# Optimization experiments

Hardware: AMD Instinct MI355X
Metric: run time of the kernel (lower is better)

Reference implementation:

```python
import jax, jax.numpy as jnp
import numpy as np

N_NODES = 50000
N_EDGES = 800000
LATDIM = 128
HEAD = 4


def setup_inputs() -> dict:
    key = jax.random.key(0)
    k1, k2, k3, k4, k5, k6 = jax.random.split(key, 6)
    scale = 1.0 / np.sqrt(LATDIM)  # xavier-ish scale for the square projections
    return {
        "embeds": jax.random.normal(k1, (N_NODES, LATDIM), dtype=jnp.float32),
        "qW": jax.random.normal(k2, (LATDIM, LATDIM), dtype=jnp.float32) * scale,
        "kW": jax.random.normal(k3, (LATDIM, LATDIM), dtype=jnp.float32) * scale,
        "vW": jax.random.normal(k4, (LATDIM, LATDIM), dtype=jnp.float32) * scale,
        "rows": jax.random.randint(k5, (N_EDGES,), 0, N_NODES, dtype=jnp.int32),
        "cols": jax.random.randint(k6, (N_EDGES,), 0, N_NODES, dtype=jnp.int32),
    }


def reference(embeds, qW, kW, vW, rows, cols):
    n_nodes, latdim = embeds.shape
    head_dim = latdim // HEAD
    rowEmb = embeds[rows]                         # [E, D] gather by dst
    colEmb = embeds[cols]                         # [E, D] gather by src
    q = (rowEmb @ qW).reshape(-1, HEAD, head_dim)  # [E, H, Dh]
    k = (colEmb @ kW).reshape(-1, HEAD, head_dim)
    v = (colEmb @ vW).reshape(-1, HEAD, head_dim)
    att = jnp.einsum('ehd,ehd->eh', q, k)
    att = jnp.clip(att, -10.0, 10.0)
    expAtt = jnp.exp(att)                          # [E, H]
    # segment softmax denominator via scatter-add over destination nodes
    attNorm = jax.ops.segment_sum(expAtt, rows, num_segments=n_nodes)[rows]
    att = expAtt / (attNorm + 1e-8)
    res = (att[:, :, None] * v).reshape(-1, latdim)  # [E, D]
    out = jax.ops.segment_sum(res, rows, num_segments=n_nodes)  # [N, D]
    return out
```

## Files before the change

### kernel.cpp

```cpp
#include <hip/hip_runtime.h>
#include <hip/hip_bf16.h>

#define N_NODES 50000
#define N_EDGES 800000
#define LATDIM 128
#define HEAD 4
#define SLOT_CAP 96

typedef __attribute__((ext_vector_type(8))) short short8;
typedef __attribute__((ext_vector_type(4))) float floatx4;

__device__ __forceinline__ unsigned bf16_rne_bits(float x) {
    unsigned u = __builtin_bit_cast(unsigned, x);
    return (u + 0x7fffu + ((u >> 16) & 1u)) & 0xffff0000u;
}
__device__ __forceinline__ void split_bf16(float x, short& hi, short& lo) {
    unsigned hb = bf16_rne_bits(x);
    hi = (short)(hb >> 16);
    float hf = __builtin_bit_cast(float, hb);
    unsigned lb = bf16_rne_bits(x - hf);
    lo = (short)(lb >> 16);
}

#define SCAT_BLOCKS ((N_EDGES / 4 + 255) / 256)

__global__ __launch_bounds__(256) void prep_kernel(
    const float* __restrict__ qW, const float* __restrict__ kW,
    const float* __restrict__ vW,
    short* __restrict__ Whi, short* __restrict__ Wlo,
    const int* __restrict__ rows, const int* __restrict__ cols,
    int* __restrict__ cnt, int* __restrict__ slots)
{
    const int b = blockIdx.x;
    if (b < 192) {
        const int which = b >> 6;
        const float* W = (which == 0) ? qW : (which == 1) ? kW : vW;
        const int t = (b & 63) * 256 + threadIdx.x;
        const int k = t >> 7, n = t & 127;
        const int c = k >> 5, q = (k >> 3) & 3, j = k & 7;
        short hi, lo;
        split_bf16(W[k * 128 + n], hi, lo);
        const int dst = which * 16384 + ((c * 128 + n) * 4 + q) * 8 + j;
        Whi[dst] = hi;
        Wlo[dst] = lo;
    } else {
        const int t = (b - 192) * 256 + threadIdx.x;
        if (t < N_EDGES / 4) {
            int4 r = ((const int4*)rows)[t];
            int4 c = ((const int4*)cols)[t];
            int p;
            p = atomicAdd(&cnt[r.x], 1);
            if (p < SLOT_CAP) slots[(size_t)r.x * SLOT_CAP + p] = c.x;
            p = atomicAdd(&cnt[r.y], 1);
            if (p < SLOT_CAP) slots[(size_t)r.y * SLOT_CAP + p] = c.y;
            p = atomicAdd(&cnt[r.z], 1);
            if (p < SLOT_CAP) slots[(size_t)r.z * SLOT_CAP + p] = c.z;
            p = atomicAdd(&cnt[r.w], 1);
            if (p < SLOT_CAP) slots[(size_t)r.w * SLOT_CAP + p] = c.w;
        }
    }
}

#define GEMM_BLOCKS ((N_NODES + 63) / 64)
#define LDSP 136

__global__ __launch_bounds__(768) void gemm_kernel(
    const float* __restrict__ E,
    const short* __restrict__ Whi, const short* __restrict__ Wlo,
    float* __restrict__ Q, unsigned short* __restrict__ KV2)
{
    __shared__ short AhL[64 * LDSP];
    __shared__ short AlL[64 * LDSP];

    const int r_base = blockIdx.x * 64;

    for (int chnk = threadIdx.x; chnk < 2048; chnk += 768) {
        const int row = chnk >> 5, c4 = chnk & 31;
        int grow = r_base + row;
        if (grow > N_NODES - 1) grow = N_NODES - 1;
        float4 x = ((const float4*)E)[(size_t)grow * 32 + c4];
        short h0, l0, h1, l1, h2, l2, h3, l3;
        split_bf16(x.x, h0, l0);
        split_bf16(x.y, h1, l1);
        split_bf16(x.z, h2, l2);
        split_bf16(x.w, h3, l3);
        *(short4*)(AhL + row * LDSP + c4 * 4) = make_short4(h0, h1, h2, h3);
        *(short4*)(AlL + row * LDSP + c4 * 4) = make_short4(l0, l1, l2, l3);
    }
    __syncthreads();

    const int wave = threadIdx.x >> 6;
    const int lane = threadIdx.x & 63;
    const int which = wave >> 2;
    const int n_base = (wave & 3) * 32;
    const int ln = lane & 15;
    const int q  = lane >> 4;

    short8 Bh[2][4], Bl[2][4];
#pragma unroll
    for (int tIdx = 0; tIdx < 2; ++tIdx)
#pragma unroll
        for (int c = 0; c < 4; ++c) {
            const int off = which * 16384 +
                            ((c * 128 + n_base + tIdx * 16 + ln) * 4 + q) * 8;
            Bh[tIdx][c] = *(const short8*)(Whi + off);
            Bl[tIdx][c] = *(const short8*)(Wlo + off);
        }

    const int vs = (which == 2) ? 32 : 0;
    const int c0 = n_base + ln;
    const int c1 = n_base + 16 + ln;

    for (int rt = 0; rt < 4; ++rt) {
        const short* ah = AhL + (rt * 16 + ln) * LDSP + q * 8;
        const short* al = AlL + (rt * 16 + ln) * LDSP + q * 8;

        floatx4 acc0 = {0.f, 0.f, 0.f, 0.f};
        floatx4 acc1 = {0.f, 0.f, 0.f, 0.f};
#pragma unroll
        for (int c = 0; c < 4; ++c) {
            short8 Ah = *(const short8*)(ah + c * 32);
            short8 Al = *(const short8*)(al + c * 32);
            acc0 = __builtin_amdgcn_mfma_f32_16x16x32_bf16(Ah, Bh[0][c], acc0, 0, 0, 0);
            acc0 = __builtin_amdgcn_mfma_f32_16x16x32_bf16(Ah, Bl[0][c], acc0, 0, 0, 0);
            acc0 = __builtin_amdgcn_mfma_f32_16x16x32_bf16(Al, Bh[0][c], acc0, 0, 0, 0);
            acc1 = __builtin_amdgcn_mfma_f32_16x16x32_bf16(Ah, Bh[1][c], acc1, 0, 0, 0);
            acc1 = __builtin_amdgcn_mfma_f32_16x16x32_bf16(Ah, Bl[1][c], acc1, 0, 0, 0);
            acc1 = __builtin_amdgcn_mfma_f32_16x16x32_bf16(Al, Bh[1][c], acc1, 0, 0, 0);
        }

        const int r0 = r_base + rt * 16;
#pragma unroll
        for (int r = 0; r < 4; ++r) {
            const int row = r0 + q * 4 + r;
            if (row >= N_NODES) continue;
            if (which == 0) {
                Q[(size_t)row * 128 + c0] = acc0[r];
                Q[(size_t)row * 128 + c1] = acc1[r];
            } else {
                KV2[(size_t)row * 256 + (c0 >> 5) * 64 + (c0 & 31) + vs] =
                    (unsigned short)(bf16_rne_bits(acc0[r]) >> 16);
                KV2[(size_t)row * 256 + (c1 >> 5) * 64 + (c1 & 31) + vs] =
                    (unsigned short)(bf16_rne_bits(acc1[r]) >> 16);
            }
        }
    }
}

__global__ __launch_bounds__(256) void fused_kernel(
    const float* __restrict__ Q,
    const unsigned short* __restrict__ KV2,
    const int* __restrict__ cnt,
    const int* __restrict__ slots,
    float* __restrict__ out)
{
    const int n = blockIdx.x * 4 + (threadIdx.x >> 6);
    if (n >= N_NODES) return;
    const int lane = threadIdx.x & 63;
    const int s  = lane & 1;
    const int h  = (lane >> 1) & 3;
    const int el = lane >> 3;

    int deg = cnt[n];
    if (deg > SLOT_CAP) deg = SLOT_CAP;

    float qv[16];
    {
        const float4* qp = (const float4*)(Q + (size_t)n * 128 + h * 32 + s * 16);
#pragma unroll
        for (int j = 0; j < 4; ++j) {
            float4 t = qp[j];
            qv[4 * j + 0] = t.x; qv[4 * j + 1] = t.y;
            qv[4 * j + 2] = t.z; qv[4 * j + 3] = t.w;
        }
    }

    float acc[16];
#pragma unroll
    for (int j = 0; j < 16; ++j) acc[j] = 0.f;
    float norm = 0.f;

    const int* srow = slots + (size_t)n * SLOT_CAP;

    for (int i = 0; i < deg; i += 8) {
        const int e = i + el;
        if (e < deg) {
            const int col = srow[e];
            const unsigned short* kp = KV2 + (size_t)col * 256 + h * 64 + s * 16;
            uint4 k0 = *(const uint4*)(kp);
            uint4 k1 = *(const uint4*)(kp + 8);
            uint4 v0 = *(const uint4*)(kp + 32);
            uint4 v1 = *(const uint4*)(kp + 40);

            unsigned kw[8] = {k0.x, k0.y, k0.z, k0.w, k1.x, k1.y, k1.z, k1.w};
            float p = 0.f;
#pragma unroll
            for (int d = 0; d < 8; ++d) {
                float flo = __builtin_bit_cast(float, kw[d] << 16);
                float fhi = __builtin_bit_cast(float, kw[d] & 0xffff0000u);
                p += qv[2 * d] * flo + qv[2 * d + 1] * fhi;
            }
            p += __shfl_xor(p, 1);

            float a = expf(fminf(fmaxf(p, -10.0f), 10.0f));
            norm += a;

            unsigned vw[8] = {v0.x, v0.y, v0.z, v0.w, v1.x, v1.y, v1.z, v1.w};
#pragma unroll
            for (int d = 0; d < 8; ++d) {
                float flo = __builtin_bit_cast(float, vw[d] << 16);
                float fhi = __builtin_bit_cast(float, vw[d] & 0xffff0000u);
                acc[2 * d]     += a * flo;
                acc[2 * d + 1] += a * fhi;
            }
        }
    }

#pragma unroll
    for (int m = 8; m <= 32; m <<= 1) {
        norm += __shfl_xor(norm, m, 64);
#pragma unroll
        for (int j = 0; j < 16; ++j) acc[j] += __shfl_xor(acc[j], m, 64);
    }

    if (el == 0) {
        const float inv = 1.0f / (norm + 1e-8f);
        float4* op = (float4*)(out + (size_t)n * 128 + h * 32 + s * 16);
#pragma unroll
        for (int j = 0; j < 4; ++j)
            op[j] = make_float4(acc[4 * j] * inv, acc[4 * j + 1] * inv,
                                acc[4 * j + 2] * inv, acc[4 * j + 3] * inv);
    }
}

extern "C" void kernel_launch(void* const* d_in, const int* in_sizes, int n_in,
                              void* d_out, int out_size, void* d_ws, size_t ws_size,
                              hipStream_t stream) {
    const float* embeds = (const float*)d_in[0];
    const float* qW     = (const float*)d_in[1];
    const float* kW     = (const float*)d_in[2];
    const float* vW     = (const float*)d_in[3];
    const int*   rows   = (const int*)d_in[4];
    const int*   cols   = (const int*)d_in[5];
    float* out = (float*)d_out;

    float* Q = (float*)d_ws;
    unsigned short* KV2 = (unsigned short*)(Q + (size_t)N_NODES * LATDIM);
    int* cnt   = (int*)(KV2 + (size_t)N_NODES * 256);
    int* slots = cnt + N_NODES;
    short* Whi = (short*)(slots + (size_t)N_NODES * SLOT_CAP);
    short* Wlo = Whi + 3 * 16384;

    hipMemsetAsync(cnt, 0, sizeof(int) * N_NODES, stream);

    prep_kernel<<<192 + SCAT_BLOCKS, 256, 0, stream>>>(
        qW, kW, vW, Whi, Wlo, rows, cols, cnt, slots);

    gemm_kernel<<<GEMM_BLOCKS, 768, 0, stream>>>(embeds, Whi, Wlo, Q, KV2);

    fused_kernel<<<(N_NODES + 3) / 4, 256, 0, stream>>>(
        Q, KV2, cnt, slots, out);
}
```

Measured before the change: 210.8 us.

## Fuse edge-scatter and projection GEMM into one kernel, splitting weights inline

```diff
diff --git a/kernel.cpp b/kernel.cpp
--- a/kernel.cpp
+++ b/kernel.cpp
@@ -6,6 +6,10 @@
 #define LATDIM 128
 #define HEAD 4
 #define SLOT_CAP 96
+
+#define SCAT_BLOCKS ((N_EDGES / 4 + 767) / 768)
+#define GEMM_BLOCKS ((N_NODES + 63) / 64)
+#define LDSP 136
 
 typedef __attribute__((ext_vector_type(8))) short short8;
 typedef __attribute__((ext_vector_type(4))) float floatx4;
@@ -22,29 +26,19 @@
     lo = (short)(lb >> 16);
 }
 
-#define SCAT_BLOCKS ((N_EDGES / 4 + 255) / 256)
-
-__global__ __launch_bounds__(256) void prep_kernel(
+__global__ __launch_bounds__(768) void mega_kernel(
+    const float* __restrict__ E,
     const float* __restrict__ qW, const float* __restrict__ kW,
     const float* __restrict__ vW,
-    short* __restrict__ Whi, short* __restrict__ Wlo,
     const int* __restrict__ rows, const int* __restrict__ cols,
-    int* __restrict__ cnt, int* __restrict__ slots)
+    int* __restrict__ cnt, int* __restrict__ slots,
+    float* __restrict__ Q, unsigned short* __restrict__ KV2)
 {
-    const int b = blockIdx.x;
-    if (b < 192) {
-        const int which = b >> 6;
-        const float* W = (which == 0) ? qW : (which == 1) ? kW : vW;
-        const int t = (b & 63) * 256 + threadIdx.x;
-        const int k = t >> 7, n = t & 127;
-        const int c = k >> 5, q = (k >> 3) & 3, j = k & 7;
-        short hi, lo;
-        split_bf16(W[k * 128 + n], hi, lo);
-        const int dst = which * 16384 + ((c * 128 + n) * 4 + q) * 8 + j;
-        Whi[dst] = hi;
-        Wlo[dst] = lo;
-    } else {
-        const int t = (b - 192) * 256 + threadIdx.x;
+    __shared__ short AhL[64 * LDSP];
+    __shared__ short AlL[64 * LDSP];
+
+    if (blockIdx.x < SCAT_BLOCKS) {
+        const int t = blockIdx.x * 768 + threadIdx.x;
         if (t < N_EDGES / 4) {
             int4 r = ((const int4*)rows)[t];
             int4 c = ((const int4*)cols)[t];
@@ -58,21 +52,10 @@
             p = atomicAdd(&cnt[r.w], 1);
             if (p < SLOT_CAP) slots[(size_t)r.w * SLOT_CAP + p] = c.w;
         }
-    }
-}
-
-#define GEMM_BLOCKS ((N_NODES + 63) / 64)
-#define LDSP 136
-
-__global__ __launch_bounds__(768) void gemm_kernel(
-    const float* __restrict__ E,
-    const short* __restrict__ Whi, const short* __restrict__ Wlo,
-    float* __restrict__ Q, unsigned short* __restrict__ KV2)
-{
-    __shared__ short AhL[64 * LDSP];
-    __shared__ short AlL[64 * LDSP];
-
-    const int r_base = blockIdx.x * 64;
+        return;
+    }
+
+    const int r_base = (blockIdx.x - SCAT_BLOCKS) * 64;
 
     for (int chnk = threadIdx.x; chnk < 2048; chnk += 768) {
         const int row = chnk >> 5, c4 = chnk & 31;
@@ -87,7 +70,6 @@
         *(short4*)(AhL + row * LDSP + c4 * 4) = make_short4(h0, h1, h2, h3);
         *(short4*)(AlL + row * LDSP + c4 * 4) = make_short4(l0, l1, l2, l3);
     }
-    __syncthreads();
 
     const int wave = threadIdx.x >> 6;
     const int lane = threadIdx.x & 63;
@@ -96,16 +78,23 @@
     const int ln = lane & 15;
     const int q  = lane >> 4;
 
+    const float* Wsrc = (which == 0) ? qW : (which == 1) ? kW : vW;
     short8 Bh[2][4], Bl[2][4];
 #pragma unroll
     for (int tIdx = 0; tIdx < 2; ++tIdx)
 #pragma unroll
         for (int c = 0; c < 4; ++c) {
-            const int off = which * 16384 +
-                            ((c * 128 + n_base + tIdx * 16 + ln) * 4 + q) * 8;
-            Bh[tIdx][c] = *(const short8*)(Whi + off);
-            Bl[tIdx][c] = *(const short8*)(Wlo + off);
-        }
+            short hv[8], lv[8];
+#pragma unroll
+            for (int j = 0; j < 8; ++j) {
+                float w = Wsrc[(c * 32 + q * 8 + j) * 128 + n_base + tIdx * 16 + ln];
+                split_bf16(w, hv[j], lv[j]);
+            }
+            Bh[tIdx][c] = *(short8*)hv;
+            Bl[tIdx][c] = *(short8*)lv;
+        }
+
+    __syncthreads();
 
     const int vs = (which == 2) ? 32 : 0;
     const int c0 = n_base + ln;
@@ -248,15 +237,11 @@
     unsigned short* KV2 = (unsigned short*)(Q + (size_t)N_NODES * LATDIM);
     int* cnt   = (int*)(KV2 + (size_t)N_NODES * 256);
     int* slots = cnt + N_NODES;
-    short* Whi = (short*)(slots + (size_t)N_NODES * SLOT_CAP);
-    short* Wlo = Whi + 3 * 16384;
 
     hipMemsetAsync(cnt, 0, sizeof(int) * N_NODES, stream);
 
-    prep_kernel<<<192 + SCAT_BLOCKS, 256, 0, stream>>>(
-        qW, kW, vW, Whi, Wlo, rows, cols, cnt, slots);
-
-    gemm_kernel<<<GEMM_BLOCKS, 768, 0, stream>>>(embeds, Whi, Wlo, Q, KV2);
+    mega_kernel<<<SCAT_BLOCKS + GEMM_BLOCKS, 768, 0, stream>>>(
+        embeds, qW, kW, vW, rows, cols, cnt, slots, Q, KV2);
 
     fused_kernel<<<(N_NODES + 3) / 4, 256, 0, stream>>>(
         Q, KV2, cnt, slots, out);
```

After: 212.0 us. No clear change (+0.6%).
